# Optimization experiments

Hardware: AMD Instinct MI355X
Metric: run time of the kernel (lower is better)

The kernel has to match this reference:

```python
import jax, jax.numpy as jnp
import numpy as np

D_MODEL = 1024
N_HEADS = 16
D_FF = 4096
DEPTH = D_MODEL // N_HEADS
EPS = 1e-5


def setup_inputs() -> dict:
    key = jax.random.key(0)
    ks = jax.random.split(key, 16)
    s = 0.02
    inp = {
        'x': jax.random.normal(ks[0], (4, 2048, D_MODEL), jnp.float32),
        'wq': jax.random.normal(ks[1], (D_MODEL, D_MODEL), jnp.float32) * s,
        'bq': jnp.zeros((D_MODEL,), jnp.float32),
        'wk': jax.random.normal(ks[2], (D_MODEL, D_MODEL), jnp.float32) * s,
        'bk': jnp.zeros((D_MODEL,), jnp.float32),
        'wv': jax.random.normal(ks[3], (D_MODEL, D_MODEL), jnp.float32) * s,
        'bv': jnp.zeros((D_MODEL,), jnp.float32),
        'wo': jax.random.normal(ks[4], (D_MODEL, D_MODEL), jnp.float32) * s,
        'bo': jnp.zeros((D_MODEL,), jnp.float32),
        'w1': jax.random.normal(ks[5], (D_MODEL, D_FF), jnp.float32) * s,
        'b1': jnp.zeros((D_FF,), jnp.float32),
        'w2': jax.random.normal(ks[6], (D_FF, D_MODEL), jnp.float32) * s,
        'b2': jnp.zeros((D_MODEL,), jnp.float32),
        'g1': jnp.ones((D_MODEL,), jnp.float32),
        'be1': jnp.zeros((D_MODEL,), jnp.float32),
        'g2': jnp.ones((D_MODEL,), jnp.float32),
        'be2': jnp.zeros((D_MODEL,), jnp.float32),
    }
    return inp


def _layernorm(x, g, b):
    mu = jnp.mean(x, -1, keepdims=True)
    var = jnp.mean((x - mu) ** 2, -1, keepdims=True)
    return (x - mu) * jax.lax.rsqrt(var + EPS) * g + b


def _rope_angles(seq_len):
    # NB: original module uses raw angles (no cos/sin applied) -- replicate faithfully
    inv_freq = 1.0 / (10000.0 ** (jnp.arange(0, DEPTH, 2, dtype=jnp.float32) / DEPTH))
    freqs = jnp.arange(seq_len, dtype=jnp.float32)[:, None] * inv_freq[None, :]  # [S, DEPTH/2]
    emb = jnp.concatenate([freqs, freqs], axis=-1)  # [S, DEPTH]
    return emb[..., 0::2], emb[..., 1::2]  # 'cos', 'sin' each [S, DEPTH/2]


def _apply_rope(t, cos, sin):
    tc, ts = t[..., 0::2], t[..., 1::2]
    return jnp.concatenate([tc * cos - ts * sin, tc * sin + ts * cos], axis=-1)


def reference(x, wq, bq, wk, bk, wv, bv, wo, bo, w1, b1, w2, b2, g1, be1, g2, be2):
    B, S, D = x.shape
    H, Dh = N_HEADS, DEPTH

    def heads(t):  # [B,S,D] -> [B,H,S,Dh]
        return t.reshape(B, S, H, Dh).transpose(0, 2, 1, 3)

    q = heads(x @ wq + bq)
    k = heads(x @ wk + bk)
    v = heads(x @ wv + bv)

    cos, sin = _rope_angles(S)  # broadcast over [B,H,S,Dh/2]
    q_rot = _apply_rope(q, cos, sin)
    k_rot = _apply_rope(k, cos, sin)

    logits = jnp.einsum('bhqd,bhkd->bhqk', q_rot, k_rot) / jnp.sqrt(jnp.float32(Dh))
    attn = jax.nn.softmax(logits, axis=-1)
    ctx = jnp.einsum('bhqk,bhkd->bhqd', attn, v)  # [B,H,S,Dh]
    ctx = ctx.transpose(0, 2, 1, 3).reshape(B, S, D)
    attn_out = ctx @ wo + bo

    h = _layernorm(x + attn_out, g1, be1)
    ff = jax.nn.relu(h @ w1 + b1) @ w2 + b2
    return _layernorm(h + ff, g2, be2)
```

## Files before the change

kernel.cpp:

```cpp
#include <hip/hip_runtime.h>

typedef _Float16 f16x8 __attribute__((ext_vector_type(8)));
typedef float    f32x4 __attribute__((ext_vector_type(4)));
typedef float    f32x2 __attribute__((ext_vector_type(2)));
typedef short    bf16x8 __attribute__((ext_vector_type(8)));

__device__ __forceinline__ float b2f(ushort u){
  union { float f; unsigned int i; } v; v.i = ((unsigned int)u) << 16; return v.f;
}
__device__ __forceinline__ ushort f2b(float f){
  union { float f; unsigned int i; } v; v.f = f;
  unsigned int r = (v.i + 0x7FFFu + ((v.i >> 16) & 1u)) >> 16;
  return (ushort)r;
}
__device__ __forceinline__ ushort f2h_u(float f){
  union { _Float16 h; ushort u; } v; v.h = (_Float16)f; return v.u;
}
__device__ __forceinline__ float ldf(const void* p, size_t i, int f){
  return f ? ((const float*)p)[i] : b2f(((const ushort*)p)[i]);
}
__device__ __forceinline__ void gld16(const void* g, void* l)
{
  __builtin_amdgcn_global_load_lds(
      (const __attribute__((address_space(1))) void*)g,
      (__attribute__((address_space(3))) void*)l, 16, 0, 0);
}

__global__ void detect_k(const void* __restrict__ x, int* __restrict__ flag)
{
  const int lane = threadIdx.x;
  const ushort* p = (const ushort*)x;
  int wild = 0, zeven = 0;
#pragma unroll
  for (int j = 0; j < 8; ++j) {
    const int idx = lane * 8 + j;
    const ushort u = p[idx];
    if (((u >> 7) & 0xFF) >= 0xF1) ++wild;
    if (((idx & 1) == 0) && u == 0) ++zeven;
  }
#pragma unroll
  for (int off = 1; off < 64; off <<= 1) {
    wild += __shfl_xor(wild, off);
    zeven += __shfl_xor(zeven, off);
  }
  if (lane == 0) *flag = (wild >= 4 || zeven >= 128) ? 1 : 0;
}

__global__ void wtab_k(float* __restrict__ w, int* __restrict__ zeroc,
                       unsigned* __restrict__ ovc)
{
  const int d = threadIdx.x;
  const int i = (d >> 1) & 15;
  const double F2 = pow(10000.0, -(double)i / 8.0);
  const double G2 = pow(10000.0, -(double)(2 * i + 1) / 16.0);
  w[d] = (float)((F2 + G2) * 0.125);
  if (d == 0) { *zeroc = 0; *ovc = 0u; }
}

__global__ __launch_bounds__(256) void cvt_wT_k(const void* __restrict__ W,
    const int* __restrict__ fp, _Float16* __restrict__ Wt, int K, int N)
{
  __shared__ float t[32][33];
  const int f = *fp;
  const int n0 = blockIdx.x * 32, k0 = blockIdx.y * 32;
  const int ln = threadIdx.x & 31, lr = threadIdx.x >> 5;
#pragma unroll
  for (int u = 0; u < 4; ++u) {
    const int kk = lr + u * 8;
    t[kk][ln] = ldf(W, (size_t)(k0 + kk) * N + n0 + ln, f);
  }
  __syncthreads();
#pragma unroll
  for (int u = 0; u < 4; ++u) {
    const int nn = lr + u * 8;
    Wt[(size_t)(n0 + nn) * K + k0 + ln] = (_Float16)t[ln][nn];
  }
}

template<int MODE>
__global__ __launch_bounds__(256) void sgemm2(
    const void* __restrict__ A, const int* __restrict__ afp,
    const void* __restrict__ W, const void* __restrict__ bias,
    const int* __restrict__ wfp,
    ushort* __restrict__ outU, float* __restrict__ outF,
    const float* __restrict__ wtab,
    int N, int K)
{
  __shared__ float As[16][128];
  __shared__ float Ws[16][132];
  const int tid = threadIdx.x;
  const int tx = tid & 15, ty = tid >> 4;
  const int bn = blockIdx.x * 128, bm = blockIdx.y * 128;
  const int af = *afp, wf = *wfp;

  float acc[8][8] = {};

  for (int k0 = 0; k0 < K; k0 += 16) {
    __syncthreads();
    {
      const int row = tid >> 1, kk0 = (tid & 1) * 8;
      float tmp[8];
      if (af) {
        const float4* p = (const float4*)((const float*)A + (size_t)(bm + row) * K + k0 + kk0);
        const float4 a = p[0], b = p[1];
        tmp[0]=a.x; tmp[1]=a.y; tmp[2]=a.z; tmp[3]=a.w;
        tmp[4]=b.x; tmp[5]=b.y; tmp[6]=b.z; tmp[7]=b.w;
      } else {
        const uint4 u = *(const uint4*)((const ushort*)A + (size_t)(bm + row) * K + k0 + kk0);
        tmp[0]=b2f((ushort)(u.x&0xffff)); tmp[1]=b2f((ushort)(u.x>>16));
        tmp[2]=b2f((ushort)(u.y&0xffff)); tmp[3]=b2f((ushort)(u.y>>16));
        tmp[4]=b2f((ushort)(u.z&0xffff)); tmp[5]=b2f((ushort)(u.z>>16));
        tmp[6]=b2f((ushort)(u.w&0xffff)); tmp[7]=b2f((ushort)(u.w>>16));
      }
#pragma unroll
      for (int u = 0; u < 8; ++u) As[kk0 + u][row] = tmp[u];
    }
    {
      const int kk = tid >> 4, c0 = (tid & 15) * 8;
      float tmp[8];
      if (wf) {
        const float4* p = (const float4*)((const float*)W + (size_t)(k0 + kk) * N + bn + c0);
        const float4 a = p[0], b = p[1];
        tmp[0]=a.x; tmp[1]=a.y; tmp[2]=a.z; tmp[3]=a.w;
        tmp[4]=b.x; tmp[5]=b.y; tmp[6]=b.z; tmp[7]=b.w;
      } else {
        const uint4 u = *(const uint4*)((const ushort*)W + (size_t)(k0 + kk) * N + bn + c0);
        tmp[0]=b2f((ushort)(u.x&0xffff)); tmp[1]=b2f((ushort)(u.x>>16));
        tmp[2]=b2f((ushort)(u.y&0xffff)); tmp[3]=b2f((ushort)(u.y>>16));
        tmp[4]=b2f((ushort)(u.z&0xffff)); tmp[5]=b2f((ushort)(u.z>>16));
        tmp[6]=b2f((ushort)(u.w&0xffff)); tmp[7]=b2f((ushort)(u.w>>16));
      }
      *(float4*)&Ws[kk][c0]     = make_float4(tmp[0], tmp[1], tmp[2], tmp[3]);
      *(float4*)&Ws[kk][c0 + 4] = make_float4(tmp[4], tmp[5], tmp[6], tmp[7]);
    }
    __syncthreads();
#pragma unroll
    for (int kk = 0; kk < 16; ++kk) {
      float ar[8], wr[8];
      const float4 a0 = *(const float4*)&As[kk][ty * 8];
      const float4 a1 = *(const float4*)&As[kk][ty * 8 + 4];
      ar[0]=a0.x; ar[1]=a0.y; ar[2]=a0.z; ar[3]=a0.w;
      ar[4]=a1.x; ar[5]=a1.y; ar[6]=a1.z; ar[7]=a1.w;
      const float4 w0 = *(const float4*)&Ws[kk][tx * 8];
      const float4 w1 = *(const float4*)&Ws[kk][tx * 8 + 4];
      wr[0]=w0.x; wr[1]=w0.y; wr[2]=w0.z; wr[3]=w0.w;
      wr[4]=w1.x; wr[5]=w1.y; wr[6]=w1.z; wr[7]=w1.w;
#pragma unroll
      for (int i = 0; i < 8; ++i)
#pragma unroll
        for (int j = 0; j < 8; ++j) acc[i][j] += ar[i] * wr[j];
    }
  }

#pragma unroll
  for (int i = 0; i < 8; ++i) {
    const int gr = bm + ty * 8 + i;
    const int b = gr >> 11, s = gr & 2047;
#pragma unroll
    for (int j = 0; j < 8; ++j) {
      const int gc = bn + tx * 8 + j;
      float v = acc[i][j] + ldf(bias, gc, wf);
      const int hh = gc >> 6, dh = gc & 63;
      const size_t idx = (size_t)b * 2097152 + (((size_t)hh * 2048) + s) * 64 + dh;
      if (MODE == 0)      outF[idx] = v * wtab[dh];
      else if (MODE == 1) outF[idx] = v;
      else                outU[idx] = f2b(v);
    }
  }
}

template<int MODE>
__global__ __launch_bounds__(256) void sgemm(
    const void* __restrict__ A, const int* __restrict__ afp, int arow0,
    const void* __restrict__ W, const void* __restrict__ bias,
    const int* __restrict__ wfp,
    const void* __restrict__ res, const int* __restrict__ rfp,
    ushort* __restrict__ outU, float* __restrict__ outF,
    const float* __restrict__ wtab,
    int N, int K, int erow0)
{
  __shared__ float As[64][17];
  __shared__ float Ws[16][65];
  const int tid = threadIdx.x;
  const int tx = tid & 15, ty = tid >> 4;
  const int bn = blockIdx.x * 64, bm = blockIdx.y * 64;
  const int af = *afp, wf = *wfp;

  float acc[4][4] = {};

  for (int k0 = 0; k0 < K; k0 += 16) {
    __syncthreads();
#pragma unroll
    for (int u = 0; u < 4; ++u) {
      const int idx = tid * 4 + u;
      const int row = idx >> 4, kk = idx & 15;
      As[row][kk] = ldf(A, (size_t)(arow0 + bm + row) * K + k0 + kk, af);
    }
#pragma unroll
    for (int u = 0; u < 4; ++u) {
      const int idx = tid * 4 + u;
      const int kk = idx >> 6, col = idx & 63;
      Ws[kk][col] = ldf(W, (size_t)(k0 + kk) * N + bn + col, wf);
    }
    __syncthreads();
#pragma unroll
    for (int kk = 0; kk < 16; ++kk) {
      float ar[4], wr[4];
#pragma unroll
      for (int i = 0; i < 4; ++i) ar[i] = As[ty * 4 + i][kk];
#pragma unroll
      for (int j = 0; j < 4; ++j) wr[j] = Ws[kk][tx * 4 + j];
#pragma unroll
      for (int i = 0; i < 4; ++i)
#pragma unroll
        for (int j = 0; j < 4; ++j) acc[i][j] += ar[i] * wr[j];
    }
  }

  const int rf = (MODE >= 4) ? *rfp : 0;
#pragma unroll
  for (int i = 0; i < 4; ++i) {
    const int gr = erow0 + bm + ty * 4 + i;
#pragma unroll
    for (int j = 0; j < 4; ++j) {
      const int gc = bn + tx * 4 + j;
      float v = acc[i][j] + ldf(bias, gc, wf);
      if (MODE == 0) {
        const int hh = gc >> 6, dh = gc & 63, s = gr & 2047;
        outF[(((size_t)hh * 2048) + s) * 64 + dh] = v * wtab[dh];
      } else if (MODE == 1) {
        const int hh = gc >> 6, dh = gc & 63, s = gr & 2047;
        outF[(((size_t)hh * 2048) + s) * 64 + dh] = v;
      } else if (MODE == 2) {
        const int hh = gc >> 6, dh = gc & 63, s = gr & 2047;
        outU[(((size_t)hh * 2048) + s) * 64 + dh] = f2b(v);
      } else if (MODE == 3) {
        outU[(size_t)gr * N + gc] = f2b(fmaxf(v, 0.f));
      } else if (MODE == 4) {
        v += ldf(res, (size_t)gr * 1024 + gc, rf);
        outU[(size_t)gr * 1024 + gc] = f2b(v);
      } else {
        v += ldf(res, (size_t)gr * 1024 + gc, rf);
        outF[(size_t)gr * 1024 + gc] = v;
      }
    }
  }
}

template<int MODE, int TM>
__global__ __launch_bounds__(256) void hgemm(
    const _Float16* __restrict__ A, int arow0,
    const _Float16* __restrict__ Wt,
    const void* __restrict__ bias, const int* __restrict__ bfp,
    const void* __restrict__ res, const int* __restrict__ rfp,
    const _Float16* __restrict__ resH,
    _Float16* __restrict__ outH, float* __restrict__ outF,
    int N, int K, int erow0)
{
  constexpr int MF = TM / 32;
  __shared__ _Float16 As[TM][32];
  __shared__ _Float16 Bs[128][32];
  const int tid = threadIdx.x;
  const int lane = tid & 63;
  const int w = tid >> 6;
  const int wm = w >> 1, wn = w & 1;
  const int fr = lane & 15, g = lane >> 4;
  const int bn = blockIdx.x * 128, bm = blockIdx.y * TM;

  f32x4 acc[MF][4];
#pragma unroll
  for (int m = 0; m < MF; ++m)
#pragma unroll
    for (int n = 0; n < 4; ++n)
      acc[m][n][0] = acc[m][n][1] = acc[m][n][2] = acc[m][n][3] = 0.f;

  for (int k0 = 0; k0 < K; k0 += 32) {
    __syncthreads();
    if constexpr (TM == 128) {
#pragma unroll
      for (int i = 0; i < 2; ++i) {
        const int c = (w * 2 + i) * 64 + lane;
        gld16(A + (size_t)(arow0 + bm + (c >> 2)) * K + k0 + (c & 3) * 8,
              (char*)As + (w * 2 + i) * 1024);
      }
    } else {
      const int c = w * 64 + lane;
      gld16(A + (size_t)(arow0 + bm + (c >> 2)) * K + k0 + (c & 3) * 8,
            (char*)As + w * 1024);
    }
#pragma unroll
    for (int i = 0; i < 2; ++i) {
      const int c = (w * 2 + i) * 64 + lane;
      gld16(Wt + (size_t)(bn + (c >> 2)) * K + k0 + (c & 3) * 8,
            (char*)Bs + (w * 2 + i) * 1024);
    }
    __syncthreads();
    f16x8 af[MF], bf8[4];
#pragma unroll
    for (int m = 0; m < MF; ++m)
      af[m] = *(const f16x8*)&As[wm * (TM / 2) + m * 16 + fr][g * 8];
#pragma unroll
    for (int n = 0; n < 4; ++n)
      bf8[n] = *(const f16x8*)&Bs[wn * 64 + n * 16 + fr][g * 8];
#pragma unroll
    for (int m = 0; m < MF; ++m)
#pragma unroll
      for (int n = 0; n < 4; ++n)
        acc[m][n] = __builtin_amdgcn_mfma_f32_16x16x32_f16(af[m], bf8[n], acc[m][n], 0, 0, 0);
  }

  const int bfl = *bfp;
  const int rfl = (MODE == 4) ? *rfp : 0;
#pragma unroll
  for (int m = 0; m < MF; ++m) {
#pragma unroll
    for (int n = 0; n < 4; ++n) {
      const int gc = bn + wn * 64 + n * 16 + fr;
      const float bv = ldf(bias, gc, bfl);
#pragma unroll
      for (int e = 0; e < 4; ++e) {
        const int gr = erow0 + bm + wm * (TM / 2) + m * 16 + (lane >> 4) * 4 + e;
        float v = acc[m][n][e] + bv;
        if (MODE == 3) {
          outH[(size_t)gr * N + gc] = (_Float16)fmaxf(v, 0.f);
        } else if (MODE == 4) {
          v += ldf(res, (size_t)gr * 1024 + gc, rfl);
          outH[(size_t)gr * 1024 + gc] = (_Float16)v;
        } else {
          v += (float)resH[(size_t)gr * 1024 + gc];
          outF[(size_t)gr * 1024 + gc] = v;
        }
      }
    }
  }
}

#define ACAP 48

__global__ __launch_bounds__(256) void attn_mfma_k(
    const float* __restrict__ qb, const float* __restrict__ kb,
    const ushort* __restrict__ vb, ushort* __restrict__ ctx,
    unsigned* __restrict__ ovcount, unsigned* __restrict__ ovlist)
{
  __shared__ __align__(16) char smem[32768];
  ushort*   kpl  = (ushort*)smem;
  unsigned* cnt  = (unsigned*)(smem + 13824);
  float*    mrow = (float*)(smem + 14080);
  ushort*   cL   = (ushort*)(smem + 14336);
  float*    LL   = (float*)(smem + 20480);

  const int tid  = threadIdx.x;
  const int lane = tid & 63;
  const int wv   = tid >> 6;
  const int fr   = lane & 15, g = lane >> 4;
  const int h = blockIdx.y, b = blockIdx.z;
  const int s0 = blockIdx.x * 64;
  const size_t bh = (size_t)b * 16 + h;
  const float*  qh = qb + bh * (2048 * 64);
  const float*  kh = kb + bh * (2048 * 64);
  const ushort* vh = vb + bh * (2048 * 64);

  {
    ushort* qs = (ushort*)smem;
    const int r = tid >> 2, d0 = (tid & 3) * 16;
    const float4* qp = (const float4*)(qh + (size_t)(s0 + r) * 64 + d0);
    float tv[16];
#pragma unroll
    for (int u = 0; u < 4; ++u) {
      const float4 t = qp[u];
      tv[u*4]=t.x; tv[u*4+1]=t.y; tv[u*4+2]=t.z; tv[u*4+3]=t.w;
    }
    ushort p0[16], p1[16], p2[16];
#pragma unroll
    for (int u = 0; u < 16; ++u) {
      const float v = tv[u];
      const ushort a0 = f2b(v);
      const float r1 = v - b2f(a0);
      const ushort a1 = f2b(r1);
      const float r2 = r1 - b2f(a1);
      p0[u]=a0; p1[u]=a1; p2[u]=f2b(r2);
    }
    const int base = r * 72 + d0;
#pragma unroll
    for (int u = 0; u < 2; ++u) {
      *(uint4*)&qs[0*4608 + base + u*8] = *(uint4*)&p0[u*8];
      *(uint4*)&qs[1*4608 + base + u*8] = *(uint4*)&p1[u*8];
      *(uint4*)&qs[2*4608 + base + u*8] = *(uint4*)&p2[u*8];
    }
  }
  __syncthreads();
  bf16x8 af[3][2];
  {
    ushort* qs = (ushort*)smem;
    const int rb = (wv * 16 + fr) * 72 + g * 8;
#pragma unroll
    for (int p = 0; p < 3; ++p)
#pragma unroll
      for (int dg = 0; dg < 2; ++dg)
        af[p][dg] = *(bf16x8*)&qs[p*4608 + rb + dg*32];
  }
  __syncthreads();
  if (tid < 64) cnt[tid] = 0;

  float svv[4];
#pragma unroll
  for (int e = 0; e < 4; ++e) svv[e] = (float)(s0 + wv * 16 + g * 4 + e);

  float mloc[4] = {-3.0e38f, -3.0e38f, -3.0e38f, -3.0e38f};

  for (int c0 = 0; c0 < 2048; c0 += 32) {
    __syncthreads();
    {
      const int key = tid >> 3, d0 = (tid & 7) * 8;
      const float4* kp4 = (const float4*)(kh + (size_t)(c0 + key) * 64 + d0);
      const float4 t0 = kp4[0], t1 = kp4[1];
      float tv[8] = {t0.x,t0.y,t0.z,t0.w,t1.x,t1.y,t1.z,t1.w};
      ushort p0[8], p1[8], p2[8];
#pragma unroll
      for (int u = 0; u < 8; ++u) {
        const float v = tv[u];
        const ushort a0 = f2b(v);
        const float r1 = v - b2f(a0);
        const ushort a1 = f2b(r1);
        const float r2 = r1 - b2f(a1);
        p0[u]=a0; p1[u]=a1; p2[u]=f2b(r2);
      }
      const int base = key * 72 + d0;
      *(uint4*)&kpl[0*2304 + base] = *(uint4*)&p0[0];
      *(uint4*)&kpl[1*2304 + base] = *(uint4*)&p1[0];
      *(uint4*)&kpl[2*2304 + base] = *(uint4*)&p2[0];
    }
    __syncthreads();

    float Lv[2][4];
#pragma unroll
    for (int kg = 0; kg < 2; ++kg) {
      f32x4 a0v = {0.f,0.f,0.f,0.f}, a1v = {0.f,0.f,0.f,0.f}, a2v = {0.f,0.f,0.f,0.f};
#pragma unroll
      for (int dg = 0; dg < 2; ++dg) {
        const int rb = (kg * 16 + fr) * 72 + dg * 32 + g * 8;
        const bf16x8 b0 = *(bf16x8*)&kpl[0*2304 + rb];
        const bf16x8 b1 = *(bf16x8*)&kpl[1*2304 + rb];
        const bf16x8 b2 = *(bf16x8*)&kpl[2*2304 + rb];
        a0v = __builtin_amdgcn_mfma_f32_16x16x32_bf16(af[0][dg], b0, a0v, 0,0,0);
        a1v = __builtin_amdgcn_mfma_f32_16x16x32_bf16(af[0][dg], b1, a1v, 0,0,0);
        a2v = __builtin_amdgcn_mfma_f32_16x16x32_bf16(af[1][dg], b0, a2v, 0,0,0);
        a0v = __builtin_amdgcn_mfma_f32_16x16x32_bf16(af[1][dg], b1, a0v, 0,0,0);
        a1v = __builtin_amdgcn_mfma_f32_16x16x32_bf16(af[0][dg], b2, a1v, 0,0,0);
        a2v = __builtin_amdgcn_mfma_f32_16x16x32_bf16(af[2][dg], b0, a2v, 0,0,0);
      }
      const float cw = (float)(c0 + kg * 16 + fr);
#pragma unroll
      for (int e = 0; e < 4; ++e) {
        const float a = (a0v[e] + a1v[e]) + a2v[e];
        Lv[kg][e] = a * cw * svv[e];
      }
    }
#pragma unroll
    for (int e = 0; e < 4; ++e) {
      float t = fmaxf(Lv[0][e], Lv[1][e]);
#pragma unroll
      for (int off = 1; off < 16; off <<= 1) t = fmaxf(t, __shfl_xor(t, off));
      mloc[e] = fmaxf(mloc[e], t);
    }
#pragma unroll
    for (int kg = 0; kg < 2; ++kg)
#pragma unroll
      for (int e = 0; e < 4; ++e) {
        if (Lv[kg][e] > mloc[e] - 80.f) {
          const int row = wv * 16 + g * 4 + e;
          const unsigned idx = atomicAdd(&cnt[row], 1u);
          if (idx < ACAP) {
            cL[row * ACAP + idx] = (ushort)(c0 + kg * 16 + fr);
            LL[row * ACAP + idx] = Lv[kg][e];
          }
        }
      }
  }
  if (fr == 0) {
#pragma unroll
    for (int e = 0; e < 4; ++e) mrow[wv * 16 + g * 4 + e] = mloc[e];
  }
  __syncthreads();

  const int row = tid >> 2, seg = tid & 3;
  const unsigned n = cnt[row];
  const int gs = s0 + row;
  if (n > ACAP) {
    if (seg == 0) {
      const unsigned i = atomicAdd(ovcount, 1u);
      ovlist[i] = (unsigned)(bh * 2048 + gs);
    }
  } else {
    const float mf = mrow[row];
    float o[16];
#pragma unroll
    for (int u = 0; u < 16; ++u) o[u] = 0.f;
    float l = 0.f;
    for (unsigned i = 0; i < n; ++i) {
      const float d = LL[row * ACAP + i] - mf;
      if (d > -80.f) {
        const int c = cL[row * ACAP + i];
        const float p = expf(d);
        l += p;
        const uint4* vp = (const uint4*)(vh + (size_t)c * 64 + seg * 16);
        const uint4 t0 = vp[0], t1 = vp[1];
        const uint wds[8] = {t0.x,t0.y,t0.z,t0.w,t1.x,t1.y,t1.z,t1.w};
#pragma unroll
        for (int u = 0; u < 8; ++u) {
          o[u*2]   += p * b2f((ushort)(wds[u] & 0xffff));
          o[u*2+1] += p * b2f((ushort)(wds[u] >> 16));
        }
      }
    }
    const float inv = 1.f / l;
    ushort* op = ctx + (((size_t)b * 2048) + gs) * 1024 + h * 64 + seg * 16;
    uint pk[8];
#pragma unroll
    for (int u = 0; u < 8; ++u)
      pk[u] = (uint)f2h_u(o[2*u] * inv) | ((uint)f2h_u(o[2*u+1] * inv) << 16);
    *(uint4*)(op)     = make_uint4(pk[0], pk[1], pk[2], pk[3]);
    *(uint4*)(op + 8) = make_uint4(pk[4], pk[5], pk[6], pk[7]);
  }
}

__global__ __launch_bounds__(256) void attn_cleanup2_k(
    const float* __restrict__ qb, const float* __restrict__ kb,
    const ushort* __restrict__ vb, ushort* __restrict__ ctx,
    const unsigned* __restrict__ ovcount, const unsigned* __restrict__ ovlist)
{
  __shared__ float Ls[2048];
  __shared__ float osum[32][65];
  __shared__ float wm[4], wl[4];
  const unsigned count = *ovcount;
  const int tid = threadIdx.x;
  const int seg = tid & 7;
  const int kq  = tid >> 3;
  const int wave = tid >> 6;

  for (unsigned idx = blockIdx.x; idx < count; idx += gridDim.x) {
    const unsigned r = ovlist[idx];
    const int gs = (int)(r & 2047u);
    const size_t bh = (size_t)(r >> 11);
    const int b = (int)(bh >> 4), h = (int)(bh & 15);
    const float*  qh = qb + bh * (2048 * 64);
    const float*  kh = kb + bh * (2048 * 64);
    const ushort* vh = vb + bh * (2048 * 64);

    float q[8];
    {
      const float4* qp = (const float4*)(qh + (size_t)gs * 64 + seg * 8);
      const float4 t0 = qp[0], t1 = qp[1];
      q[0]=t0.x; q[1]=t0.y; q[2]=t0.z; q[3]=t0.w;
      q[4]=t1.x; q[5]=t1.y; q[6]=t1.z; q[7]=t1.w;
    }
    const float sq = (float)gs;

    float mloc = -3.0e38f;
    for (int it = 0; it < 64; ++it) {
      const int c = it * 32 + kq;
      const float4* kp = (const float4*)(kh + (size_t)c * 64 + seg * 8);
      const float4 a = kp[0], bb = kp[1];
      float dt = q[0]*a.x + q[1]*a.y + q[2]*a.z + q[3]*a.w
               + q[4]*bb.x + q[5]*bb.y + q[6]*bb.z + q[7]*bb.w;
      dt += __shfl_xor(dt, 1);
      dt += __shfl_xor(dt, 2);
      dt += __shfl_xor(dt, 4);
      const float L = dt * sq * (float)c;
      if (seg == 0) Ls[c] = L;
      mloc = fmaxf(mloc, L);
    }
    mloc = fmaxf(mloc, __shfl_xor(mloc, 8));
    mloc = fmaxf(mloc, __shfl_xor(mloc, 16));
    mloc = fmaxf(mloc, __shfl_xor(mloc, 32));
    if ((tid & 63) == 0) wm[wave] = mloc;
    __syncthreads();
    const float m = fmaxf(fmaxf(wm[0], wm[1]), fmaxf(wm[2], wm[3]));

    float o[8] = {0.f,0.f,0.f,0.f,0.f,0.f,0.f,0.f};
    float lloc = 0.f;
    for (int it = 0; it < 64; ++it) {
      const int c = it * 32 + kq;
      const float p = expf(Ls[c] - m);
      lloc += p;
      const uint4 vv = *(const uint4*)(vh + (size_t)c * 64 + seg * 8);
      o[0] += p * b2f((ushort)(vv.x & 0xffff)); o[1] += p * b2f((ushort)(vv.x >> 16));
      o[2] += p * b2f((ushort)(vv.y & 0xffff)); o[3] += p * b2f((ushort)(vv.y >> 16));
      o[4] += p * b2f((ushort)(vv.z & 0xffff)); o[5] += p * b2f((ushort)(vv.z >> 16));
      o[6] += p * b2f((ushort)(vv.w & 0xffff)); o[7] += p * b2f((ushort)(vv.w >> 16));
    }
    lloc += __shfl_xor(lloc, 8);
    lloc += __shfl_xor(lloc, 16);
    lloc += __shfl_xor(lloc, 32);
    if ((tid & 63) == 0) wl[wave] = lloc;
#pragma unroll
    for (int u = 0; u < 8; ++u) osum[kq][seg * 8 + u] = o[u];
    __syncthreads();
    const float l = (wl[0] + wl[1]) + (wl[2] + wl[3]);
    if (tid < 64) {
      float acc = 0.f;
#pragma unroll
      for (int k2 = 0; k2 < 32; ++k2) acc += osum[k2][tid];
      ctx[(((size_t)b * 2048) + gs) * 1024 + h * 64 + tid] = f2h_u(acc / l);
    }
    __syncthreads();
  }
}

template<int RPT, int OF16>
__global__ __launch_bounds__(256) void attn_k(
    const float* __restrict__ qb, const float* __restrict__ kb,
    const ushort* __restrict__ vb, ushort* __restrict__ ctx,
    int b0, size_t bstrF, size_t bstrU)
{
  __shared__ float kS[64][64];
  __shared__ float vS[64][64];
  const int tid = threadIdx.x;
  const int h  = blockIdx.y;
  const int bz = blockIdx.z;
  const int b  = b0 + bz;
  const float*  qh = qb + bstrF * bz + (size_t)h * 2048 * 64;
  const float*  kh = kb + bstrF * bz + (size_t)h * 2048 * 64;
  const ushort* vh = vb + bstrU * bz + (size_t)h * 2048 * 64;

  const int seg  = tid & 3;
  const int slot = tid >> 2;
  const int row0 = blockIdx.x * (64 * RPT) + slot * RPT;

  f32x2 qv[RPT][8], o[RPT][8];
  float m[RPT], l[RPT], sq[RPT];
#pragma unroll
  for (int i = 0; i < RPT; ++i) {
    const float4* qp = (const float4*)(qh + (size_t)(row0 + i) * 64 + seg * 16);
#pragma unroll
    for (int w = 0; w < 4; ++w) {
      const float4 t = qp[w];
      qv[i][2*w]   = f32x2{t.x, t.y};
      qv[i][2*w+1] = f32x2{t.z, t.w};
    }
    m[i] = -3.0e38f; l[i] = 0.f; sq[i] = (float)(row0 + i);
#pragma unroll
    for (int t = 0; t < 8; ++t) o[i][t] = f32x2{0.f, 0.f};
  }

  for (int c0 = 0; c0 < 2048; c0 += 64) {
    __syncthreads();
    {
      const int key = tid >> 2, sg = tid & 3;
      const float4* sp = (const float4*)(kh + (size_t)(c0 + key) * 64 + sg * 16);
      float4* dp = (float4*)&kS[key][sg * 16];
#pragma unroll
      for (int u = 0; u < 4; ++u) dp[u] = sp[u];
      const uint4* vp = (const uint4*)(vh + (size_t)(c0 + key) * 64 + sg * 16);
      float* vd = &vS[key][sg * 16];
#pragma unroll
      for (int u = 0; u < 2; ++u) {
        const uint4 t = vp[u];
        vd[u*8+0] = b2f((ushort)(t.x & 0xffff)); vd[u*8+1] = b2f((ushort)(t.x >> 16));
        vd[u*8+2] = b2f((ushort)(t.y & 0xffff)); vd[u*8+3] = b2f((ushort)(t.y >> 16));
        vd[u*8+4] = b2f((ushort)(t.z & 0xffff)); vd[u*8+5] = b2f((ushort)(t.z >> 16));
        vd[u*8+6] = b2f((ushort)(t.w & 0xffff)); vd[u*8+7] = b2f((ushort)(t.w >> 16));
      }
    }
    __syncthreads();
#pragma unroll 2
    for (int j = 0; j < 64; ++j) {
      const float4* kp = (const float4*)&kS[j][seg * 16];
      const float4 ka = kp[0], kb4 = kp[1], kc = kp[2], kd = kp[3];
      const f32x2 K0 = {ka.x, ka.y},  K1 = {ka.z, ka.w};
      const f32x2 K2 = {kb4.x, kb4.y}, K3 = {kb4.z, kb4.w};
      const f32x2 K4 = {kc.x, kc.y},  K5 = {kc.z, kc.w};
      const f32x2 K6 = {kd.x, kd.y},  K7 = {kd.z, kd.w};
      float dt[RPT];
#pragma unroll
      for (int i = 0; i < RPT; ++i) {
        f32x2 a2 = qv[i][0] * K0;
        a2 += qv[i][1] * K1;
        a2 += qv[i][2] * K2;
        a2 += qv[i][3] * K3;
        a2 += qv[i][4] * K4;
        a2 += qv[i][5] * K5;
        a2 += qv[i][6] * K6;
        a2 += qv[i][7] * K7;
        dt[i] = a2[0] + a2[1];
      }
#pragma unroll
      for (int i = 0; i < RPT; ++i) {
        dt[i] += __shfl_xor(dt[i], 1);
        dt[i] += __shfl_xor(dt[i], 2);
      }
      const float cc = (float)(c0 + j);
#pragma unroll
      for (int i = 0; i < RPT; ++i) {
        const float L = dt[i] * sq[i] * cc;
        const float d = L - m[i];
        if (d > 0.f) {
          const float r = expf(-d);
          l[i] = l[i] * r + 1.f;
          m[i] = L;
          const f32x2 r2 = {r, r};
          const float4* vp4 = (const float4*)&vS[j][seg * 16];
          const float4 va = vp4[0], vb4 = vp4[1], vc = vp4[2], vd4 = vp4[3];
          const f32x2 V[8] = {{va.x,va.y},{va.z,va.w},{vb4.x,vb4.y},{vb4.z,vb4.w},
                              {vc.x,vc.y},{vc.z,vc.w},{vd4.x,vd4.y},{vd4.z,vd4.w}};
#pragma unroll
          for (int t = 0; t < 8; ++t) o[i][t] = o[i][t] * r2 + V[t];
        } else if (d > -80.f) {
          const float p = expf(d);
          l[i] += p;
          const f32x2 p2 = {p, p};
          const float4* vp4 = (const float4*)&vS[j][seg * 16];
          const float4 va = vp4[0], vb4 = vp4[1], vc = vp4[2], vd4 = vp4[3];
          const f32x2 V[8] = {{va.x,va.y},{va.z,va.w},{vb4.x,vb4.y},{vb4.z,vb4.w},
                              {vc.x,vc.y},{vc.z,vc.w},{vd4.x,vd4.y},{vd4.z,vd4.w}};
#pragma unroll
          for (int t = 0; t < 8; ++t) o[i][t] += p2 * V[t];
        }
      }
    }
  }

#pragma unroll
  for (int i = 0; i < RPT; ++i) {
    const float inv = 1.f / l[i];
    ushort* op = ctx + (((size_t)b * 2048) + row0 + i) * 1024 + h * 64 + seg * 16;
    uint pk[8];
#pragma unroll
    for (int t2 = 0; t2 < 8; ++t2) {
      const uint lo = OF16 ? (uint)f2h_u(o[i][t2][0] * inv) : (uint)f2b(o[i][t2][0] * inv);
      const uint hi = OF16 ? (uint)f2h_u(o[i][t2][1] * inv) : (uint)f2b(o[i][t2][1] * inv);
      pk[t2] = lo | (hi << 16);
    }
    *(uint4*)(op)     = make_uint4(pk[0], pk[1], pk[2], pk[3]);
    *(uint4*)(op + 8) = make_uint4(pk[4], pk[5], pk[6], pk[7]);
  }
}

__global__ __launch_bounds__(256) void ln_k(const ushort* __restrict__ y,
                                            const void* __restrict__ g,
                                            const void* __restrict__ be,
                                            const int* __restrict__ fp,
                                            ushort* __restrict__ out)
{
  const int row = blockIdx.x, tid = threadIdx.x;
  const int f = *fp;
  const ushort* p = y + (size_t)row * 1024;
  float v[4], s = 0.f, s2 = 0.f;
#pragma unroll
  for (int i = 0; i < 4; ++i) {
    const float x = b2f(p[tid + i * 256]);
    v[i] = x; s += x; s2 += x * x;
  }
#pragma unroll
  for (int off = 1; off < 64; off <<= 1) { s += __shfl_xor(s, off); s2 += __shfl_xor(s2, off); }
  __shared__ float red[8];
  const int wave = tid >> 6, lane = tid & 63;
  if (lane == 0) { red[wave] = s; red[4 + wave] = s2; }
  __syncthreads();
  s = red[0] + red[1] + red[2] + red[3];
  s2 = red[4] + red[5] + red[6] + red[7];
  const float mu = s * (1.f / 1024.f);
  const float var = s2 * (1.f / 1024.f) - mu * mu;
  const float rstd = rsqrtf(var + 1e-5f);
  ushort* o = out + (size_t)row * 1024;
#pragma unroll
  for (int i = 0; i < 4; ++i) {
    const int c = tid + i * 256;
    o[c] = f2b((v[i] - mu) * rstd * ldf(g, c, f) + ldf(be, c, f));
  }
}

__global__ __launch_bounds__(256) void ln_h_k(const _Float16* __restrict__ y,
                                              const void* __restrict__ g,
                                              const void* __restrict__ be,
                                              const int* __restrict__ fp,
                                              _Float16* __restrict__ out)
{
  const int row = blockIdx.x, tid = threadIdx.x;
  const int f = *fp;
  const _Float16* p = y + (size_t)row * 1024;
  float v[4], s = 0.f, s2 = 0.f;
#pragma unroll
  for (int i = 0; i < 4; ++i) {
    const float x = (float)p[tid + i * 256];
    v[i] = x; s += x; s2 += x * x;
  }
#pragma unroll
  for (int off = 1; off < 64; off <<= 1) { s += __shfl_xor(s, off); s2 += __shfl_xor(s2, off); }
  __shared__ float red[8];
  const int wave = tid >> 6, lane = tid & 63;
  if (lane == 0) { red[wave] = s; red[4 + wave] = s2; }
  __syncthreads();
  s = red[0] + red[1] + red[2] + red[3];
  s2 = red[4] + red[5] + red[6] + red[7];
  const float mu = s * (1.f / 1024.f);
  const float var = s2 * (1.f / 1024.f) - mu * mu;
  const float rstd = rsqrtf(var + 1e-5f);
  _Float16* o = out + (size_t)row * 1024;
#pragma unroll
  for (int i = 0; i < 4; ++i) {
    const int c = tid + i * 256;
    o[c] = (_Float16)((v[i] - mu) * rstd * ldf(g, c, f) + ldf(be, c, f));
  }
}

__global__ __launch_bounds__(256) void ln_f32_k(float* __restrict__ y,
                                                const void* __restrict__ g,
                                                const void* __restrict__ be,
                                                const int* __restrict__ fp)
{
  const int row = blockIdx.x, tid = threadIdx.x;
  const int f = *fp;
  float* p = y + (size_t)row * 1024;
  float v[4], s = 0.f, s2 = 0.f;
#pragma unroll
  for (int i = 0; i < 4; ++i) {
    const float x = p[tid + i * 256];
    v[i] = x; s += x; s2 += x * x;
  }
#pragma unroll
  for (int off = 1; off < 64; off <<= 1) { s += __shfl_xor(s, off); s2 += __shfl_xor(s2, off); }
  __shared__ float red[8];
  const int wave = tid >> 6, lane = tid & 63;
  if (lane == 0) { red[wave] = s; red[4 + wave] = s2; }
  __syncthreads();
  s = red[0] + red[1] + red[2] + red[3];
  s2 = red[4] + red[5] + red[6] + red[7];
  const float mu = s * (1.f / 1024.f);
  const float var = s2 * (1.f / 1024.f) - mu * mu;
  const float rstd = rsqrtf(var + 1e-5f);
#pragma unroll
  for (int i = 0; i < 4; ++i) {
    const int c = tid + i * 256;
    p[c] = (v[i] - mu) * rstd * ldf(g, c, f) + ldf(be, c, f);
  }
}

extern "C" void kernel_launch(void* const* d_in, const int* in_sizes, int n_in,
                              void* d_out, int out_size, void* d_ws, size_t ws_size,
                              hipStream_t stream)
{
  const void* x  = d_in[0];
  const void* wq = d_in[1];  const void* bq = d_in[2];
  const void* wk = d_in[3];  const void* bk = d_in[4];
  const void* wv = d_in[5];  const void* bv = d_in[6];
  const void* wo = d_in[7];  const void* bo = d_in[8];
  const void* w1 = d_in[9];  const void* b1 = d_in[10];
  const void* w2 = d_in[11]; const void* b2 = d_in[12];
  const void* g1 = d_in[13]; const void* be1 = d_in[14];
  const void* g2 = d_in[15]; const void* be2 = d_in[16];
  float* outp = (float*)d_out;

  const size_t MB = 1048576;
  char* ws = (char*)d_ws;
  int*      flag    = (int*)(ws + 0);
  int*      zeroc   = (int*)(ws + 64);
  unsigned* ovcount = (unsigned*)(ws + 128);
  float*    wtab    = (float*)(ws + 256);

  detect_k<<<dim3(1), dim3(64), 0, stream>>>(x, flag);
  wtab_k<<<dim3(1), dim3(64), 0, stream>>>(wtab, zeroc, ovcount);

  const size_t QS = (size_t)16 * 2048 * 64;

  if (ws_size >= (size_t)98 * MB) {
    float*     qb   = (float*)(ws + 1 * MB);
    float*     kb   = (float*)(ws + 33 * MB);
    ushort*    vb   = (ushort*)(ws + 65 * MB);
    ushort*    ctxh = (ushort*)(ws + 81 * MB);
    unsigned*  ovlist = (unsigned*)(ws + 97 * MB);
    _Float16*  WoT  = (_Float16*)(ws + 65 * MB);
    _Float16*  W1T  = (_Float16*)(ws + 67 * MB);
    _Float16*  W2T  = (_Float16*)(ws + 75 * MB);
    _Float16*  y1h  = (_Float16*)(ws + 1 * MB);
    _Float16*  hh   = (_Float16*)(ws + 17 * MB);
    _Float16*  ffc  = (_Float16*)(ws + 33 * MB);

    sgemm2<0><<<dim3(8, 64), 256, 0, stream>>>(x, flag, wq, bq, flag,
                                               nullptr, qb, wtab, 1024, 1024);
    sgemm2<1><<<dim3(8, 64), 256, 0, stream>>>(x, flag, wk, bk, flag,
                                               nullptr, kb, wtab, 1024, 1024);
    sgemm2<2><<<dim3(8, 64), 256, 0, stream>>>(x, flag, wv, bv, flag,
                                               vb, nullptr, wtab, 1024, 1024);

    attn_mfma_k<<<dim3(32, 16, 4), 256, 0, stream>>>(qb, kb, vb, ctxh,
                                                     ovcount, ovlist);
    attn_cleanup2_k<<<dim3(8192), 256, 0, stream>>>(qb, kb, vb, ctxh,
                                                    ovcount, ovlist);

    cvt_wT_k<<<dim3(32, 32),  256, 0, stream>>>(wo, flag, WoT, 1024, 1024);
    cvt_wT_k<<<dim3(128, 32), 256, 0, stream>>>(w1, flag, W1T, 1024, 4096);

    hgemm<4, 128><<<dim3(8, 64), 256, 0, stream>>>((const _Float16*)ctxh, 0, WoT,
                                                   bo, flag, x, flag, nullptr,
                                                   y1h, nullptr, 1024, 1024, 0);
    cvt_wT_k<<<dim3(32, 128), 256, 0, stream>>>(w2, flag, W2T, 4096, 1024);

    ln_h_k<<<dim3(8192), 256, 0, stream>>>(y1h, g1, be1, flag, hh);

    for (int c = 0; c < 2; ++c) {
      hgemm<3, 128><<<dim3(32, 32), 256, 0, stream>>>(hh, c * 4096, W1T,
                                                      b1, flag, nullptr, zeroc, nullptr,
                                                      ffc, nullptr, 4096, 1024, 0);
      hgemm<5, 64><<<dim3(8, 64), 256, 0, stream>>>(ffc, 0, W2T,
                                                    b2, flag, nullptr, zeroc, hh,
                                                    nullptr, outp, 1024, 4096, c * 4096);
    }
    ln_f32_k<<<dim3(8192), 256, 0, stream>>>(outp, g2, be2, flag);
  } else {
    float*  qb   = (float*)(ws + 1 * MB);
    float*  kb   = (float*)(ws + 9 * MB);
    ushort* vb   = (ushort*)(ws + 17 * MB);
    ushort* ctxb = (ushort*)(ws + 22 * MB);
    ushort* y1   = (ushort*)(ws + 1 * MB);
    ushort* hbuf = (ushort*)(ws + 22 * MB);
    ushort* ffc  = (ushort*)(ws + 1 * MB);

    for (int b = 0; b < 4; ++b) {
      sgemm<0><<<dim3(16, 32), 256, 0, stream>>>(x, flag, b * 2048, wq, bq, flag,
                                                 nullptr, nullptr, nullptr, qb, wtab,
                                                 1024, 1024, b * 2048);
      sgemm<1><<<dim3(16, 32), 256, 0, stream>>>(x, flag, b * 2048, wk, bk, flag,
                                                 nullptr, nullptr, nullptr, kb, wtab,
                                                 1024, 1024, b * 2048);
      sgemm<2><<<dim3(16, 32), 256, 0, stream>>>(x, flag, b * 2048, wv, bv, flag,
                                                 nullptr, nullptr, vb, nullptr, wtab,
                                                 1024, 1024, b * 2048);
      attn_k<1, 0><<<dim3(32, 16, 1), 256, 0, stream>>>(qb, kb, vb, ctxb, b, 0, 0);
    }

    sgemm<4><<<dim3(16, 128), 256, 0, stream>>>(ctxb, zeroc, 0, wo, bo, flag,
                                                x, flag, y1, nullptr, wtab,
                                                1024, 1024, 0);
    ln_k<<<dim3(8192), 256, 0, stream>>>(y1, g1, be1, flag, hbuf);
    for (int c = 0; c < 4; ++c) {
      sgemm<3><<<dim3(64, 32), 256, 0, stream>>>(hbuf, zeroc, c * 2048, w1, b1, flag,
                                                 nullptr, nullptr, ffc, nullptr, wtab,
                                                 4096, 1024, 0);
      sgemm<5><<<dim3(16, 32), 256, 0, stream>>>(ffc, zeroc, 0, w2, b2, flag,
                                                 hbuf, zeroc, nullptr, outp, wtab,
                                                 1024, 4096, c * 2048);
    }
    ln_f32_k<<<dim3(8192), 256, 0, stream>>>(outp, g2, be2, flag);
  }
}
```

Measured before the change: 1.546 ms.

## Double-buffer hgemm LDS tiles and process 128 query rows per attention block

The fp16 GEMM now double-buffers its A/B LDS tiles, issuing the next k-slice's global-to-LDS loads before the MFMAs on the current slice, with one barrier per iteration instead of two. The attention kernel handles 128 query rows per block instead of 64, so each K tile converted to the three-way bf16 split is reused across twice as many queries and the grid is halved. The costs are more registers for the doubled Q fragments and accumulators, a larger shared-memory footprint that may lower occupancy, and fewer blocks in the attention launch.

```diff
diff --git a/kernel.cpp b/kernel.cpp
--- a/kernel.cpp
+++ b/kernel.cpp
@@ -258,8 +258,8 @@
     int N, int K, int erow0)
 {
   constexpr int MF = TM / 32;
-  __shared__ _Float16 As[TM][32];
-  __shared__ _Float16 Bs[128][32];
+  __shared__ _Float16 As[2][TM][32];
+  __shared__ _Float16 Bs[2][128][32];
   const int tid = threadIdx.x;
   const int lane = tid & 63;
   const int w = tid >> 6;
@@ -274,39 +274,46 @@
     for (int n = 0; n < 4; ++n)
       acc[m][n][0] = acc[m][n][1] = acc[m][n][2] = acc[m][n][3] = 0.f;
 
-  for (int k0 = 0; k0 < K; k0 += 32) {
-    __syncthreads();
+  auto STAGE = [&](int buf, int k0) {
     if constexpr (TM == 128) {
 #pragma unroll
       for (int i = 0; i < 2; ++i) {
         const int c = (w * 2 + i) * 64 + lane;
         gld16(A + (size_t)(arow0 + bm + (c >> 2)) * K + k0 + (c & 3) * 8,
-              (char*)As + (w * 2 + i) * 1024);
+              (char*)As[buf] + (w * 2 + i) * 1024);
       }
     } else {
       const int c = w * 64 + lane;
       gld16(A + (size_t)(arow0 + bm + (c >> 2)) * K + k0 + (c & 3) * 8,
-            (char*)As + w * 1024);
+            (char*)As[buf] + w * 1024);
     }
 #pragma unroll
     for (int i = 0; i < 2; ++i) {
       const int c = (w * 2 + i) * 64 + lane;
       gld16(Wt + (size_t)(bn + (c >> 2)) * K + k0 + (c & 3) * 8,
-            (char*)Bs + (w * 2 + i) * 1024);
-    }
-    __syncthreads();
-    f16x8 af[MF], bf8[4];
+            (char*)Bs[buf] + (w * 2 + i) * 1024);
+    }
+  };
+
+  STAGE(0, 0);
+  __syncthreads();
+  int cur = 0;
+  for (int k0 = 0; k0 < K; k0 += 32) {
+    if (k0 + 32 < K) STAGE(cur ^ 1, k0 + 32);
+    f16x8 afr[MF], bf8[4];
 #pragma unroll
     for (int m = 0; m < MF; ++m)
-      af[m] = *(const f16x8*)&As[wm * (TM / 2) + m * 16 + fr][g * 8];
+      afr[m] = *(const f16x8*)&As[cur][wm * (TM / 2) + m * 16 + fr][g * 8];
 #pragma unroll
     for (int n = 0; n < 4; ++n)
-      bf8[n] = *(const f16x8*)&Bs[wn * 64 + n * 16 + fr][g * 8];
+      bf8[n] = *(const f16x8*)&Bs[cur][wn * 64 + n * 16 + fr][g * 8];
 #pragma unroll
     for (int m = 0; m < MF; ++m)
 #pragma unroll
       for (int n = 0; n < 4; ++n)
-        acc[m][n] = __builtin_amdgcn_mfma_f32_16x16x32_f16(af[m], bf8[n], acc[m][n], 0, 0, 0);
+        acc[m][n] = __builtin_amdgcn_mfma_f32_16x16x32_f16(afr[m], bf8[n], acc[m][n], 0, 0, 0);
+    __syncthreads();
+    cur ^= 1;
   }
 
   const int bfl = *bfp;
@@ -342,71 +349,82 @@
     const ushort* __restrict__ vb, ushort* __restrict__ ctx,
     unsigned* __restrict__ ovcount, unsigned* __restrict__ ovlist)
 {
-  __shared__ __align__(16) char smem[32768];
+  __shared__ __align__(16) char smem[51712];
   ushort*   kpl  = (ushort*)smem;
   unsigned* cnt  = (unsigned*)(smem + 13824);
-  float*    mrow = (float*)(smem + 14080);
-  ushort*   cL   = (ushort*)(smem + 14336);
-  float*    LL   = (float*)(smem + 20480);
+  float*    mrow = (float*)(smem + 14336);
+  ushort*   cL   = (ushort*)(smem + 14848);
+  float*    LL   = (float*)(smem + 27136);
 
   const int tid  = threadIdx.x;
   const int lane = tid & 63;
   const int wv   = tid >> 6;
   const int fr   = lane & 15, g = lane >> 4;
   const int h = blockIdx.y, b = blockIdx.z;
-  const int s0 = blockIdx.x * 64;
+  const int s0 = blockIdx.x * 128;
   const size_t bh = (size_t)b * 16 + h;
   const float*  qh = qb + bh * (2048 * 64);
   const float*  kh = kb + bh * (2048 * 64);
   const ushort* vh = vb + bh * (2048 * 64);
 
-  {
-    ushort* qs = (ushort*)smem;
-    const int r = tid >> 2, d0 = (tid & 3) * 16;
-    const float4* qp = (const float4*)(qh + (size_t)(s0 + r) * 64 + d0);
-    float tv[16];
-#pragma unroll
-    for (int u = 0; u < 4; ++u) {
-      const float4 t = qp[u];
-      tv[u*4]=t.x; tv[u*4+1]=t.y; tv[u*4+2]=t.z; tv[u*4+3]=t.w;
-    }
-    ushort p0[16], p1[16], p2[16];
-#pragma unroll
-    for (int u = 0; u < 16; ++u) {
-      const float v = tv[u];
-      const ushort a0 = f2b(v);
-      const float r1 = v - b2f(a0);
-      const ushort a1 = f2b(r1);
-      const float r2 = r1 - b2f(a1);
-      p0[u]=a0; p1[u]=a1; p2[u]=f2b(r2);
-    }
-    const int base = r * 72 + d0;
-#pragma unroll
-    for (int u = 0; u < 2; ++u) {
-      *(uint4*)&qs[0*4608 + base + u*8] = *(uint4*)&p0[u*8];
-      *(uint4*)&qs[1*4608 + base + u*8] = *(uint4*)&p1[u*8];
-      *(uint4*)&qs[2*4608 + base + u*8] = *(uint4*)&p2[u*8];
+  bf16x8 af[2][3][2];
+#pragma unroll
+  for (int rs = 0; rs < 2; ++rs) {
+    if (rs) __syncthreads();
+    {
+      ushort* qs = (ushort*)smem;
+      const int r = tid >> 2, d0 = (tid & 3) * 16;
+      const float4* qp = (const float4*)(qh + (size_t)(s0 + rs * 64 + r) * 64 + d0);
+      float tv[16];
+#pragma unroll
+      for (int u = 0; u < 4; ++u) {
+        const float4 t = qp[u];
+        tv[u*4]=t.x; tv[u*4+1]=t.y; tv[u*4+2]=t.z; tv[u*4+3]=t.w;
+      }
+      ushort p0[16], p1[16], p2[16];
+#pragma unroll
+      for (int u = 0; u < 16; ++u) {
+        const float v = tv[u];
+        const ushort a0 = f2b(v);
+        const float r1 = v - b2f(a0);
+        const ushort a1 = f2b(r1);
+        const float r2 = r1 - b2f(a1);
+        p0[u]=a0; p1[u]=a1; p2[u]=f2b(r2);
+      }
+      const int base = r * 72 + d0;
+#pragma unroll
+      for (int u = 0; u < 2; ++u) {
+        *(uint4*)&((ushort*)smem)[0*4608 + base + u*8] = *(uint4*)&p0[u*8];
+        *(uint4*)&((ushort*)smem)[1*4608 + base + u*8] = *(uint4*)&p1[u*8];
+        *(uint4*)&((ushort*)smem)[2*4608 + base + u*8] = *(uint4*)&p2[u*8];
+      }
+    }
+    __syncthreads();
+    {
+      ushort* qs = (ushort*)smem;
+      const int rb = (wv * 16 + fr) * 72 + g * 8;
+#pragma unroll
+      for (int p = 0; p < 3; ++p)
+#pragma unroll
+        for (int dg = 0; dg < 2; ++dg)
+          af[rs][p][dg] = *(bf16x8*)&qs[p*4608 + rb + dg*32];
     }
   }
   __syncthreads();
-  bf16x8 af[3][2];
-  {
-    ushort* qs = (ushort*)smem;
-    const int rb = (wv * 16 + fr) * 72 + g * 8;
-#pragma unroll
-    for (int p = 0; p < 3; ++p)
-#pragma unroll
-      for (int dg = 0; dg < 2; ++dg)
-        af[p][dg] = *(bf16x8*)&qs[p*4608 + rb + dg*32];
-  }
-  __syncthreads();
-  if (tid < 64) cnt[tid] = 0;
-
-  float svv[4];
-#pragma unroll
-  for (int e = 0; e < 4; ++e) svv[e] = (float)(s0 + wv * 16 + g * 4 + e);
-
-  float mloc[4] = {-3.0e38f, -3.0e38f, -3.0e38f, -3.0e38f};
+  if (tid < 128) cnt[tid] = 0;
+
+  float svv[2][4];
+#pragma unroll
+  for (int rs = 0; rs < 2; ++rs)
+#pragma unroll
+    for (int e = 0; e < 4; ++e)
+      svv[rs][e] = (float)(s0 + rs * 64 + wv * 16 + g * 4 + e);
+
+  float mloc[2][4];
+#pragma unroll
+  for (int rs = 0; rs < 2; ++rs)
+#pragma unroll
+    for (int e = 0; e < 4; ++e) mloc[rs][e] = -3.0e38f;
 
   for (int c0 = 0; c0 < 2048; c0 += 32) {
     __syncthreads();
@@ -432,95 +450,104 @@
     }
     __syncthreads();
 
-    float Lv[2][4];
-#pragma unroll
-    for (int kg = 0; kg < 2; ++kg) {
-      f32x4 a0v = {0.f,0.f,0.f,0.f}, a1v = {0.f,0.f,0.f,0.f}, a2v = {0.f,0.f,0.f,0.f};
-#pragma unroll
-      for (int dg = 0; dg < 2; ++dg) {
-        const int rb = (kg * 16 + fr) * 72 + dg * 32 + g * 8;
-        const bf16x8 b0 = *(bf16x8*)&kpl[0*2304 + rb];
-        const bf16x8 b1 = *(bf16x8*)&kpl[1*2304 + rb];
-        const bf16x8 b2 = *(bf16x8*)&kpl[2*2304 + rb];
-        a0v = __builtin_amdgcn_mfma_f32_16x16x32_bf16(af[0][dg], b0, a0v, 0,0,0);
-        a1v = __builtin_amdgcn_mfma_f32_16x16x32_bf16(af[0][dg], b1, a1v, 0,0,0);
-        a2v = __builtin_amdgcn_mfma_f32_16x16x32_bf16(af[1][dg], b0, a2v, 0,0,0);
-        a0v = __builtin_amdgcn_mfma_f32_16x16x32_bf16(af[1][dg], b1, a0v, 0,0,0);
-        a1v = __builtin_amdgcn_mfma_f32_16x16x32_bf16(af[0][dg], b2, a1v, 0,0,0);
-        a2v = __builtin_amdgcn_mfma_f32_16x16x32_bf16(af[2][dg], b0, a2v, 0,0,0);
-      }
-      const float cw = (float)(c0 + kg * 16 + fr);
+    float Lv[2][2][4];
+#pragma unroll
+    for (int rs = 0; rs < 2; ++rs) {
+#pragma unroll
+      for (int kg = 0; kg < 2; ++kg) {
+        f32x4 a0v = {0.f,0.f,0.f,0.f}, a1v = {0.f,0.f,0.f,0.f}, a2v = {0.f,0.f,0.f,0.f};
+#pragma unroll
+        for (int dg = 0; dg < 2; ++dg) {
+          const int rb = (kg * 16 + fr) * 72 + dg * 32 + g * 8;
+          const bf16x8 b0 = *(bf16x8*)&kpl[0*2304 + rb];
+          const bf16x8 b1 = *(bf16x8*)&kpl[1*2304 + rb];
+          const bf16x8 b2 = *(bf16x8*)&kpl[2*2304 + rb];
+          a0v = __builtin_amdgcn_mfma_f32_16x16x32_bf16(af[rs][0][dg], b0, a0v, 0,0,0);
+          a1v = __builtin_amdgcn_mfma_f32_16x16x32_bf16(af[rs][0][dg], b1, a1v, 0,0,0);
+          a2v = __builtin_amdgcn_mfma_f32_16x16x32_bf16(af[rs][1][dg], b0, a2v, 0,0,0);
+          a0v = __builtin_amdgcn_mfma_f32_16x16x32_bf16(af[rs][1][dg], b1, a0v, 0,0,0);
+          a1v = __builtin_amdgcn_mfma_f32_16x16x32_bf16(af[rs][0][dg], b2, a1v, 0,0,0);
+          a2v = __builtin_amdgcn_mfma_f32_16x16x32_bf16(af[rs][2][dg], b0, a2v, 0,0,0);
+        }
+        const float cw = (float)(c0 + kg * 16 + fr);
+#pragma unroll
+        for (int e = 0; e < 4; ++e) {
+          const float a = (a0v[e] + a1v[e]) + a2v[e];
+          Lv[rs][kg][e] = a * cw * svv[rs][e];
+        }
+      }
 #pragma unroll
       for (int e = 0; e < 4; ++e) {
-        const float a = (a0v[e] + a1v[e]) + a2v[e];
-        Lv[kg][e] = a * cw * svv[e];
-      }
-    }
-#pragma unroll
-    for (int e = 0; e < 4; ++e) {
-      float t = fmaxf(Lv[0][e], Lv[1][e]);
-#pragma unroll
-      for (int off = 1; off < 16; off <<= 1) t = fmaxf(t, __shfl_xor(t, off));
-      mloc[e] = fmaxf(mloc[e], t);
-    }
-#pragma unroll
-    for (int kg = 0; kg < 2; ++kg)
-#pragma unroll
-      for (int e = 0; e < 4; ++e) {
-        if (Lv[kg][e] > mloc[e] - 80.f) {
-          const int row = wv * 16 + g * 4 + e;
-          const unsigned idx = atomicAdd(&cnt[row], 1u);
-          if (idx < ACAP) {
-            cL[row * ACAP + idx] = (ushort)(c0 + kg * 16 + fr);
-            LL[row * ACAP + idx] = Lv[kg][e];
+        float t = fmaxf(Lv[rs][0][e], Lv[rs][1][e]);
+#pragma unroll
+        for (int off = 1; off < 16; off <<= 1) t = fmaxf(t, __shfl_xor(t, off));
+        mloc[rs][e] = fmaxf(mloc[rs][e], t);
+      }
+#pragma unroll
+      for (int kg = 0; kg < 2; ++kg)
+#pragma unroll
+        for (int e = 0; e < 4; ++e) {
+          if (Lv[rs][kg][e] > mloc[rs][e] - 80.f) {
+            const int row = rs * 64 + wv * 16 + g * 4 + e;
+            const unsigned idx = atomicAdd(&cnt[row], 1u);
+            if (idx < ACAP) {
+              cL[row * ACAP + idx] = (ushort)(c0 + kg * 16 + fr);
+              LL[row * ACAP + idx] = Lv[rs][kg][e];
+            }
           }
         }
-      }
+    }
   }
   if (fr == 0) {
 #pragma unroll
-    for (int e = 0; e < 4; ++e) mrow[wv * 16 + g * 4 + e] = mloc[e];
+    for (int rs = 0; rs < 2; ++rs)
+#pragma unroll
+      for (int e = 0; e < 4; ++e)
+        mrow[rs * 64 + wv * 16 + g * 4 + e] = mloc[rs][e];
   }
   __syncthreads();
 
-  const int row = tid >> 2, seg = tid & 3;
-  const unsigned n = cnt[row];
-  const int gs = s0 + row;
-  if (n > ACAP) {
-    if (seg == 0) {
-      const unsigned i = atomicAdd(ovcount, 1u);
-      ovlist[i] = (unsigned)(bh * 2048 + gs);
-    }
-  } else {
-    const float mf = mrow[row];
-    float o[16];
-#pragma unroll
-    for (int u = 0; u < 16; ++u) o[u] = 0.f;
-    float l = 0.f;
-    for (unsigned i = 0; i < n; ++i) {
-      const float d = LL[row * ACAP + i] - mf;
-      if (d > -80.f) {
-        const int c = cL[row * ACAP + i];
-        const float p = expf(d);
-        l += p;
-        const uint4* vp = (const uint4*)(vh + (size_t)c * 64 + seg * 16);
-        const uint4 t0 = vp[0], t1 = vp[1];
-        const uint wds[8] = {t0.x,t0.y,t0.z,t0.w,t1.x,t1.y,t1.z,t1.w};
-#pragma unroll
-        for (int u = 0; u < 8; ++u) {
-          o[u*2]   += p * b2f((ushort)(wds[u] & 0xffff));
-          o[u*2+1] += p * b2f((ushort)(wds[u] >> 16));
+#pragma unroll
+  for (int rs = 0; rs < 2; ++rs) {
+    const int row = rs * 64 + (tid >> 2), seg = tid & 3;
+    const unsigned n = cnt[row];
+    const int gs = s0 + row;
+    if (n > ACAP) {
+      if (seg == 0) {
+        const unsigned i = atomicAdd(ovcount, 1u);
+        ovlist[i] = (unsigned)(bh * 2048 + gs);
+      }
+    } else {
+      const float mf = mrow[row];
+      float o[16];
+#pragma unroll
+      for (int u = 0; u < 16; ++u) o[u] = 0.f;
+      float l = 0.f;
+      for (unsigned i = 0; i < n; ++i) {
+        const float d = LL[row * ACAP + i] - mf;
+        if (d > -80.f) {
+          const int c = cL[row * ACAP + i];
+          const float p = expf(d);
+          l += p;
+          const uint4* vp = (const uint4*)(vh + (size_t)c * 64 + seg * 16);
+          const uint4 t0 = vp[0], t1 = vp[1];
+          const uint wds[8] = {t0.x,t0.y,t0.z,t0.w,t1.x,t1.y,t1.z,t1.w};
+#pragma unroll
+          for (int u = 0; u < 8; ++u) {
+            o[u*2]   += p * b2f((ushort)(wds[u] & 0xffff));
+            o[u*2+1] += p * b2f((ushort)(wds[u] >> 16));
+          }
         }
       }
-    }
-    const float inv = 1.f / l;
-    ushort* op = ctx + (((size_t)b * 2048) + gs) * 1024 + h * 64 + seg * 16;
-    uint pk[8];
-#pragma unroll
-    for (int u = 0; u < 8; ++u)
-      pk[u] = (uint)f2h_u(o[2*u] * inv) | ((uint)f2h_u(o[2*u+1] * inv) << 16);
-    *(uint4*)(op)     = make_uint4(pk[0], pk[1], pk[2], pk[3]);
-    *(uint4*)(op + 8) = make_uint4(pk[4], pk[5], pk[6], pk[7]);
+      const float inv = 1.f / l;
+      ushort* op = ctx + (((size_t)b * 2048) + gs) * 1024 + h * 64 + seg * 16;
+      uint pk[8];
+#pragma unroll
+      for (int u = 0; u < 8; ++u)
+        pk[u] = (uint)f2h_u(o[2*u] * inv) | ((uint)f2h_u(o[2*u+1] * inv) << 16);
+      *(uint4*)(op)     = make_uint4(pk[0], pk[1], pk[2], pk[3]);
+      *(uint4*)(op + 8) = make_uint4(pk[4], pk[5], pk[6], pk[7]);
+    }
   }
 }
 
@@ -883,7 +910,7 @@
     sgemm2<2><<<dim3(8, 64), 256, 0, stream>>>(x, flag, wv, bv, flag,
                                                vb, nullptr, wtab, 1024, 1024);
 
-    attn_mfma_k<<<dim3(32, 16, 4), 256, 0, stream>>>(qb, kb, vb, ctxh,
+    attn_mfma_k<<<dim3(16, 16, 4), 256, 0, stream>>>(qb, kb, vb, ctxh,
                                                      ovcount, ovlist);
     attn_cleanup2_k<<<dim3(8192), 256, 0, stream>>>(qb, kb, vb, ctxh,
                                                     ovcount, ovlist);
```

Result: no change. 1.566 ms (+1.3%).
